# Kernel optimization log

Hardware: AMD Instinct MI355X
Metric: run time of the kernel (lower is better)

The kernel has to match this reference:

```python
import jax, jax.numpy as jnp
import numpy as np

D = 1024  # embed_dim

def setup_inputs() -> dict:
    key = jax.random.key(0)
    ks = jax.random.split(key, 5)
    s = 1.0 / np.sqrt(D)  # keep weight magnitudes sane
    x = jax.random.normal(ks[0], (2, 4096, D), dtype=jnp.float32)
    Wq = jax.random.normal(ks[1], (D, D), dtype=jnp.float32) * s
    Wk = jax.random.normal(ks[2], (D, D), dtype=jnp.float32) * s
    Wv = jax.random.normal(ks[3], (D, D), dtype=jnp.float32) * s
    Wo = jax.random.normal(ks[4], (D, D), dtype=jnp.float32) * s
    return {"x": x, "Wq": Wq, "Wk": Wk, "Wv": Wv, "Wo": Wo}

def reference(x, Wq, Wk, Wv, Wo):
    # torch nn.Linear(no bias): y = x @ W.T
    q = jnp.einsum('bsd,ed->bse', x, Wq)
    k = jnp.einsum('bsd,ed->bse', x, Wk)
    v = jnp.einsum('bsd,ed->bse', x, Wv)
    embed_dim = x.shape[-1]
    scores = jnp.einsum('bqd,bkd->bqk', q, k) / jnp.sqrt(jnp.asarray(embed_dim, x.dtype))
    attn = jax.nn.softmax(scores, axis=-1)  # dropout is identity in eval mode (p=0)
    out = jnp.einsum('bqk,bkd->bqd', attn, v)
    out = jnp.einsum('bsd,ed->bse', out, Wo)
    return out
```

## Files before the change

### kernel.cpp

```cpp
#include <hip/hip_runtime.h>
#include <hip/hip_bf16.h>

using short8 = __attribute__((ext_vector_type(8))) short;
using f32x4  = __attribute__((ext_vector_type(4))) float;

__device__ __forceinline__ unsigned short f2bf(float f) {
  union { float f; unsigned int u; } x; x.f = f;
  unsigned int r = (x.u + 0x7fffu + ((x.u >> 16) & 1u)) >> 16;
  return (unsigned short)r;
}

__device__ __forceinline__ void gld_lds16(const short* gp, short* lp) {
  __builtin_amdgcn_global_load_lds((const __attribute__((address_space(1))) void*)gp,
                                   (__attribute__((address_space(3))) void*)lp, 16, 0, 0);
}

__global__ __launch_bounds__(256) void cast_all(const float* __restrict__ x,
                                                const float* __restrict__ Wq,
                                                const float* __restrict__ Wk,
                                                const float* __restrict__ Wv,
                                                const float* __restrict__ Wo,
                                                short* __restrict__ xb,
                                                short* __restrict__ U,
                                                short* __restrict__ V,
                                                float4* __restrict__ sums4) {
  const int bid = blockIdx.x;
  const int tid = threadIdx.x;
  if (bid < 9216) {
    const float4* src;
    short* dst;
    const int i = bid * 256 + tid;
    if (bid < 8192) {
      src = (const float4*)x + i;
      dst = xb + 4ll * i;
    } else {
      const int off = i - 2097152;
      src = (const float4*)Wo + off;
      dst = U + 1048576 + 4ll * off;
    }
    float4 f = *src;
    short4 o;
    o.x = (short)f2bf(f.x); o.y = (short)f2bf(f.y);
    o.z = (short)f2bf(f.z); o.w = (short)f2bf(f.w);
    *(short4*)dst = o;
    if (bid < 8) sums4[bid * 256 + tid] = float4{0.f, 0.f, 0.f, 0.f};
  } else {
    __shared__ short tls[64][65];
    const int t  = bid - 9216;
    const int w  = t >> 8;
    const int ti = t & 255;
    const int bx = ti & 15, by = ti >> 4;
    const float* src = (w == 0) ? Wq : (w == 1) ? Wk : Wv;
    short* dst = (w == 0) ? V : (w == 1) ? U : V + 1048576;
    const int r  = tid >> 4;
    const int c4 = (tid & 15) * 4;
#pragma unroll
    for (int s = 0; s < 4; ++s) {
      float4 f = *(const float4*)(src + (long long)(by * 64 + r + s * 16) * 1024 + bx * 64 + c4);
      tls[r + s * 16][c4 + 0] = (short)f2bf(f.x);
      tls[r + s * 16][c4 + 1] = (short)f2bf(f.y);
      tls[r + s * 16][c4 + 2] = (short)f2bf(f.z);
      tls[r + s * 16][c4 + 3] = (short)f2bf(f.w);
    }
    __syncthreads();
#pragma unroll
    for (int s = 0; s < 4; ++s) {
      const int a = r + s * 16;
      short4 o;
      o.x = tls[c4 + 0][a]; o.y = tls[c4 + 1][a];
      o.z = tls[c4 + 2][a]; o.w = tls[c4 + 3][a];
      *(short4*)(dst + (long long)(bx * 64 + a) * 1024 + by * 64 + c4) = o;
    }
  }
}

template <int MODE>
__global__ __launch_bounds__(256) void gemm_bt(const short* __restrict__ A,
                                               const short* __restrict__ B,
                                               void* __restrict__ Cv,
                                               float* __restrict__ sums,
                                               int K, int ldc, float scale,
                                               long long aStr, long long bStr,
                                               long long cStr, int gy, int ng) {
  __shared__ short lA[128 * 64];
  __shared__ short lB[128 * 64];
  const int bid = blockIdx.x;
  const int bx  = bid / ng;
  const int g   = bid % ng;
  const int by  = g % gy;
  const long long z = g / gy;
  const int tid = threadIdx.x;
  const int w   = tid >> 6;
  const int l   = tid & 63;
  const int wm  = w >> 1, wn = w & 1;
  const long long tm = (long long)by * 128;
  const long long tn = (long long)bx * 128;
  A += z * aStr;
  B += z * bStr;

  const bool swp = (MODE == 2) ? (bx < 8) : true;

  f32x4 acc[4][4] = {};

  const int lr   = l >> 3;
  const int scw  = ((l & 7) ^ (lr & 7)) * 8;
  const int q4   = l >> 4;
  const int fr   = l & 15;
  const int xr   = fr & 7;

  for (int k0 = 0; k0 < K; k0 += 64) {
#pragma unroll
    for (int t = 0; t < 4; ++t) {
      const int seg = w * 4 + t;
      gld_lds16(A + (tm + seg * 8 + lr) * (long long)K + k0 + scw, &lA[seg * 512]);
      gld_lds16(B + (tn + seg * 8 + lr) * (long long)K + k0 + scw, &lB[seg * 512]);
    }
    __syncthreads();
#pragma unroll
    for (int kk = 0; kk < 64; kk += 32) {
      const int cs = ((((kk >> 3)) + q4) ^ xr) << 3;
      short8 af[4], bfr[4];
#pragma unroll
      for (int i = 0; i < 4; ++i)
        af[i] = *(const short8*)&lA[(wm * 64 + i * 16 + fr) * 64 + cs];
#pragma unroll
      for (int j = 0; j < 4; ++j)
        bfr[j] = *(const short8*)&lB[(wn * 64 + j * 16 + fr) * 64 + cs];
      if (swp) {
#pragma unroll
        for (int i = 0; i < 4; ++i)
#pragma unroll
          for (int j = 0; j < 4; ++j)
            acc[i][j] = __builtin_amdgcn_mfma_f32_16x16x32_bf16(bfr[j], af[i], acc[i][j], 0, 0, 0);
      } else {
#pragma unroll
        for (int i = 0; i < 4; ++i)
#pragma unroll
          for (int j = 0; j < 4; ++j)
            acc[i][j] = __builtin_amdgcn_mfma_f32_16x16x32_bf16(af[i], bfr[j], acc[i][j], 0, 0, 0);
      }
    }
    __syncthreads();
  }

  const int rb = (l >> 4) * 4;

  if (MODE == 1) {
    unsigned short* dst = (unsigned short*)Cv + z * cStr;
#pragma unroll
    for (int i = 0; i < 4; ++i) {
      const long long row = tm + wm * 64 + i * 16 + fr;
#pragma unroll
      for (int j = 0; j < 4; ++j) {
        const long long colb = tn + wn * 64 + j * 16 + rb;
        short4 pk;
        pk.x = (short)f2bf(acc[i][j][0]); pk.y = (short)f2bf(acc[i][j][1]);
        pk.z = (short)f2bf(acc[i][j][2]); pk.w = (short)f2bf(acc[i][j][3]);
        *(short4*)(dst + row * ldc + colb) = pk;
      }
    }
  } else if (MODE == 2) {
    if (swp) {
      unsigned short* dst = (unsigned short*)Cv;
      const int cb0 = (int)tn + wn * 64;
#pragma unroll
      for (int i = 0; i < 4; ++i) {
        const long long row = tm + wm * 64 + i * 16 + fr;
#pragma unroll
        for (int j = 0; j < 4; ++j) {
          const int colb = cb0 + j * 16 + rb;
          short4 pk;
          pk.x = (short)f2bf(acc[i][j][0]); pk.y = (short)f2bf(acc[i][j][1]);
          pk.z = (short)f2bf(acc[i][j][2]); pk.w = (short)f2bf(acc[i][j][3]);
          *(short4*)(dst + row * 1024 + colb) = pk;
        }
      }
    } else {
      unsigned short* dst = (unsigned short*)Cv + 8388608ll;
      const int cb0 = (int)(tn - 1024) + wn * 64;
#pragma unroll
      for (int i = 0; i < 4; ++i)
#pragma unroll
        for (int j = 0; j < 4; ++j) {
          const long long row0 = tm + wm * 64 + i * 16 + rb;
          const long long b = row0 >> 12, s0 = row0 & 4095;
          const int c = cb0 + j * 16 + fr;
          short4 pk;
          pk.x = (short)f2bf(acc[i][j][0]); pk.y = (short)f2bf(acc[i][j][1]);
          pk.z = (short)f2bf(acc[i][j][2]); pk.w = (short)f2bf(acc[i][j][3]);
          *(short4*)(dst + b * 4194304ll + (long long)c * 4096 + s0) = pk;
        }
    }
  } else if (MODE == 4) {
    unsigned short* dst = (unsigned short*)Cv + z * cStr;
    float* sm = sums + z * 4096;
#pragma unroll
    for (int i = 0; i < 4; ++i) {
      const long long row = tm + wm * 64 + i * 16 + fr;
      float rs = 0.f;
#pragma unroll
      for (int j = 0; j < 4; ++j) {
        const long long colb = tn + wn * 64 + j * 16 + rb;
        short4 pk;
        float e0 = __expf(acc[i][j][0] * scale);
        float e1 = __expf(acc[i][j][1] * scale);
        float e2 = __expf(acc[i][j][2] * scale);
        float e3 = __expf(acc[i][j][3] * scale);
        rs += (e0 + e1) + (e2 + e3);
        pk.x = (short)f2bf(e0); pk.y = (short)f2bf(e1);
        pk.z = (short)f2bf(e2); pk.w = (short)f2bf(e3);
        *(short4*)(dst + row * ldc + colb) = pk;
      }
      rs += __shfl_xor(rs, 16);
      rs += __shfl_xor(rs, 32);
      if (l < 16) atomicAdd(sm + tm + wm * 64 + i * 16 + l, rs);
    }
  } else {
    float* dst = (float*)Cv + z * cStr;
    const float* sm = sums + z * 4096;
#pragma unroll
    for (int i = 0; i < 4; ++i) {
      const long long row = tm + wm * 64 + i * 16 + fr;
      const float inv = 1.0f / sm[row];
#pragma unroll
      for (int j = 0; j < 4; ++j) {
        const long long colb = tn + wn * 64 + j * 16 + rb;
        f32x4 o;
        o[0] = acc[i][j][0] * inv; o[1] = acc[i][j][1] * inv;
        o[2] = acc[i][j][2] * inv; o[3] = acc[i][j][3] * inv;
        *(f32x4*)(dst + row * ldc + colb) = o;
      }
    }
  }
}

extern "C" void kernel_launch(void* const* d_in, const int* in_sizes, int n_in,
                              void* d_out, int out_size, void* d_ws, size_t ws_size,
                              hipStream_t stream) {
  const float* x  = (const float*)d_in[0];
  const float* Wq = (const float*)d_in[1];
  const float* Wk = (const float*)d_in[2];
  const float* Wv = (const float*)d_in[3];
  const float* Wo = (const float*)d_in[4];
  float* out = (float*)d_out;

  char* ws = (char*)d_ws;
  short* xb = (short*)ws;
  short* U  = (short*)(ws + (16ll << 20));
  short* V  = (short*)(ws + (20ll << 20));
  short* W2 = (short*)(ws + (24ll << 20));
  short* t  = (short*)(ws + (28ll << 20));
  short* vt = t + 8388608;
  float* sums = (float*)(ws + (60ll << 20));
  short* sc = (short*)(ws + (88ll << 20));

  const bool batched = ws_size >= 159383552ull;
  dim3 blk(256);

  cast_all<<<9984, blk, 0, stream>>>(x, Wq, Wk, Wv, Wo, xb, U, V, (float4*)sums);

  gemm_bt<1><<<8 * 16, blk, 0, stream>>>(U, V, W2, nullptr, 1024, 1024, 1.f,
                                         1048576ll, 1048576ll, 1048576ll, 8, 16);

  gemm_bt<2><<<16 * 64, blk, 0, stream>>>(xb, W2, t, nullptr, 1024, 1024, 1.f,
                                          0, 0, 0, 64, 64);

  if (batched) {
    gemm_bt<4><<<32 * 64, blk, 0, stream>>>(t, xb, sc, sums, 1024, 4096, 0.03125f,
                                            4194304ll, 4194304ll, 16777216ll, 32, 64);
    gemm_bt<6><<<8 * 64, blk, 0, stream>>>(sc, vt, out, sums, 4096, 1024, 1.f,
                                           16777216ll, 4194304ll, 4194304ll, 32, 64);
  } else {
    for (int b = 0; b < 2; ++b) {
      short* tb  = t  + (long long)b * 4194304;
      short* xbb = xb + (long long)b * 4194304;
      short* vb  = vt + (long long)b * 4194304;
      float* ob  = out + (long long)b * 4194304;
      float* smb = sums + (long long)b * 4096;
      gemm_bt<4><<<32 * 32, blk, 0, stream>>>(tb, xbb, sc, smb, 1024, 4096, 0.03125f,
                                              0, 0, 0, 32, 32);
      gemm_bt<6><<<8 * 32, blk, 0, stream>>>(sc, vb, ob, smb, 4096, 1024, 1.f,
                                             0, 0, 0, 32, 32);
    }
  }
}
```

Baseline: 328.7 us.

## Add 256x256-tile 8-wave GEMM kernel for projection and score stages

Introduces a new gemm8 kernel using 512 threads, 256x256 output tiles, a 4-stage LDS ring with direct global-to-LDS loads, and MFMA 16x16x32 bf16. It replaces the 128-tile gemm_bt for the fused projection (MODE 2) and the score/exp stage (MODE 4), with epilogues for bf16 store, transposed V store, and exp with atomic row sums. Larger tiles raise arithmetic intensity and reduce global/LDS traffic per FLOP. The cost is much higher register pressure (128 accumulator floats per thread) and fewer blocks, which may limit occupancy and tail balance.

```diff
diff --git a/kernel.cpp b/kernel.cpp
--- a/kernel.cpp
+++ b/kernel.cpp
@@ -234,6 +234,171 @@
   }
 }
 
+template <int MODE>
+__global__ __launch_bounds__(512, 2) void gemm8(const short* __restrict__ A,
+                                                const short* __restrict__ B,
+                                                void* __restrict__ Cv,
+                                                float* __restrict__ sums,
+                                                int K, int ldc, float scale,
+                                                long long aStr, long long bStr,
+                                                long long cStr, int gy, int ng) {
+  __shared__ __align__(16) short lds[4][2][8192];
+  const int bid = blockIdx.x;
+  const int bx  = bid / ng;
+  const int g   = bid % ng;
+  const int by  = g % gy;
+  const long long z = g / gy;
+  const int tid = threadIdx.x;
+  const int l   = tid & 63;
+  const int w   = tid >> 6;
+  const int wm  = w >> 2, wn = w & 3;
+  const long long tm = (long long)by * 256;
+  const long long tn = (long long)bx * 256;
+  A += z * aStr;
+  B += z * bStr;
+
+  const bool swp = (MODE == 2) ? (bx < 4) : true;
+
+  f32x4 acc[8][4] = {};
+
+  const int i0 = tid, i1 = tid + 512;
+  const int r0 = i0 >> 2, q0 = i0 & 3;
+  const int r1 = i1 >> 2, q1 = i1 & 3;
+  const int sw0 = (q0 ^ ((r0 >> 1) & 3)) * 8;
+  const int sw1 = (q1 ^ ((r1 >> 1) & 3)) * 8;
+  const int db0 = (tid & 448) * 8;
+  const int db1 = 4096 + db0;
+  const short* Arow0 = A + (tm + r0) * (long long)K + sw0;
+  const short* Arow1 = A + (tm + r1) * (long long)K + sw1;
+  const short* Brow0 = B + (tn + r0) * (long long)K + sw0;
+  const short* Brow1 = B + (tn + r1) * (long long)K + sw1;
+
+  const int q4 = l >> 4;
+  const int fr = l & 15;
+  int offA[8], offB[4];
+#pragma unroll
+  for (int i = 0; i < 8; ++i) {
+    const int r = wm * 128 + i * 16 + fr;
+    offA[i] = r * 32 + ((q4 ^ ((r >> 1) & 3)) << 3);
+  }
+#pragma unroll
+  for (int j = 0; j < 4; ++j) {
+    const int r = wn * 64 + j * 16 + fr;
+    offB[j] = r * 32 + ((q4 ^ ((r >> 1) & 3)) << 3);
+  }
+
+  const int nt = K >> 5;
+
+#define STAGE8(tt)                                          \
+  {                                                         \
+    const int s_ = (tt) & 3;                                \
+    const int k_ = (tt) << 5;                               \
+    gld_lds16(Arow0 + k_, &lds[s_][0][db0]);                \
+    gld_lds16(Arow1 + k_, &lds[s_][0][db1]);                \
+    gld_lds16(Brow0 + k_, &lds[s_][1][db0]);                \
+    gld_lds16(Brow1 + k_, &lds[s_][1][db1]);                \
+  }
+
+  STAGE8(0);
+  STAGE8(1);
+  asm volatile("s_waitcnt vmcnt(4)" ::: "memory");
+  __builtin_amdgcn_s_barrier();
+
+  for (int t = 0; t < nt; ++t) {
+    if (t + 2 < nt) STAGE8(t + 2);
+    const short* sA = &lds[t & 3][0][0];
+    const short* sB = &lds[t & 3][1][0];
+    short8 bfr[4];
+#pragma unroll
+    for (int j = 0; j < 4; ++j) bfr[j] = *(const short8*)&sB[offB[j]];
+    __builtin_amdgcn_s_setprio(1);
+    if (swp) {
+#pragma unroll
+      for (int i = 0; i < 8; ++i) {
+        short8 af = *(const short8*)&sA[offA[i]];
+#pragma unroll
+        for (int j = 0; j < 4; ++j)
+          acc[i][j] = __builtin_amdgcn_mfma_f32_16x16x32_bf16(bfr[j], af, acc[i][j], 0, 0, 0);
+      }
+    } else {
+#pragma unroll
+      for (int i = 0; i < 8; ++i) {
+        short8 af = *(const short8*)&sA[offA[i]];
+#pragma unroll
+        for (int j = 0; j < 4; ++j)
+          acc[i][j] = __builtin_amdgcn_mfma_f32_16x16x32_bf16(af, bfr[j], acc[i][j], 0, 0, 0);
+      }
+    }
+    __builtin_amdgcn_s_setprio(0);
+    if (t + 1 < nt) {
+      if (t + 2 < nt) { asm volatile("s_waitcnt vmcnt(4)" ::: "memory"); }
+      else            { asm volatile("s_waitcnt vmcnt(0)" ::: "memory"); }
+      __builtin_amdgcn_s_barrier();
+    }
+  }
+#undef STAGE8
+
+  const int rb = q4 * 4;
+
+  if (MODE == 2) {
+    if (swp) {
+      unsigned short* dst = (unsigned short*)Cv;
+      const int cb0 = (int)tn + wn * 64;
+#pragma unroll
+      for (int i = 0; i < 8; ++i) {
+        const long long row = tm + wm * 128 + i * 16 + fr;
+#pragma unroll
+        for (int j = 0; j < 4; ++j) {
+          const int colb = cb0 + j * 16 + rb;
+          short4 pk;
+          pk.x = (short)f2bf(acc[i][j][0]); pk.y = (short)f2bf(acc[i][j][1]);
+          pk.z = (short)f2bf(acc[i][j][2]); pk.w = (short)f2bf(acc[i][j][3]);
+          *(short4*)(dst + row * 1024 + colb) = pk;
+        }
+      }
+    } else {
+      unsigned short* dst = (unsigned short*)Cv + 8388608ll;
+      const int cb0 = (int)(tn - 1024) + wn * 64;
+#pragma unroll
+      for (int i = 0; i < 8; ++i)
+#pragma unroll
+        for (int j = 0; j < 4; ++j) {
+          const long long row0 = tm + wm * 128 + i * 16 + rb;
+          const long long b = row0 >> 12, s0 = row0 & 4095;
+          const int c = cb0 + j * 16 + fr;
+          short4 pk;
+          pk.x = (short)f2bf(acc[i][j][0]); pk.y = (short)f2bf(acc[i][j][1]);
+          pk.z = (short)f2bf(acc[i][j][2]); pk.w = (short)f2bf(acc[i][j][3]);
+          *(short4*)(dst + b * 4194304ll + (long long)c * 4096 + s0) = pk;
+        }
+    }
+  } else {
+    unsigned short* dst = (unsigned short*)Cv + z * cStr;
+    float* sm = sums + z * 4096;
+#pragma unroll
+    for (int i = 0; i < 8; ++i) {
+      const long long row = tm + wm * 128 + i * 16 + fr;
+      float rs = 0.f;
+#pragma unroll
+      for (int j = 0; j < 4; ++j) {
+        const long long colb = tn + wn * 64 + j * 16 + rb;
+        short4 pk;
+        float e0 = __expf(acc[i][j][0] * scale);
+        float e1 = __expf(acc[i][j][1] * scale);
+        float e2 = __expf(acc[i][j][2] * scale);
+        float e3 = __expf(acc[i][j][3] * scale);
+        rs += (e0 + e1) + (e2 + e3);
+        pk.x = (short)f2bf(e0); pk.y = (short)f2bf(e1);
+        pk.z = (short)f2bf(e2); pk.w = (short)f2bf(e3);
+        *(short4*)(dst + row * ldc + colb) = pk;
+      }
+      rs += __shfl_xor(rs, 16);
+      rs += __shfl_xor(rs, 32);
+      if (l < 16) atomicAdd(sm + tm + wm * 128 + i * 16 + l, rs);
+    }
+  }
+}
+
 extern "C" void kernel_launch(void* const* d_in, const int* in_sizes, int n_in,
                               void* d_out, int out_size, void* d_ws, size_t ws_size,
                               hipStream_t stream) {
@@ -256,18 +421,19 @@
 
   const bool batched = ws_size >= 159383552ull;
   dim3 blk(256);
+  dim3 blk8(512);
 
   cast_all<<<9984, blk, 0, stream>>>(x, Wq, Wk, Wv, Wo, xb, U, V, (float4*)sums);
 
   gemm_bt<1><<<8 * 16, blk, 0, stream>>>(U, V, W2, nullptr, 1024, 1024, 1.f,
                                          1048576ll, 1048576ll, 1048576ll, 8, 16);
 
-  gemm_bt<2><<<16 * 64, blk, 0, stream>>>(xb, W2, t, nullptr, 1024, 1024, 1.f,
-                                          0, 0, 0, 64, 64);
+  gemm8<2><<<8 * 32, blk8, 0, stream>>>(xb, W2, t, nullptr, 1024, 1024, 1.f,
+                                        0, 0, 0, 32, 32);
 
   if (batched) {
-    gemm_bt<4><<<32 * 64, blk, 0, stream>>>(t, xb, sc, sums, 1024, 4096, 0.03125f,
-                                            4194304ll, 4194304ll, 16777216ll, 32, 64);
+    gemm8<4><<<16 * 32, blk8, 0, stream>>>(t, xb, sc, sums, 1024, 4096, 0.03125f,
+                                           4194304ll, 4194304ll, 16777216ll, 16, 32);
     gemm_bt<6><<<8 * 64, blk, 0, stream>>>(sc, vt, out, sums, 4096, 1024, 1.f,
                                            16777216ll, 4194304ll, 4194304ll, 32, 64);
   } else {
@@ -277,8 +443,8 @@
       short* vb  = vt + (long long)b * 4194304;
       float* ob  = out + (long long)b * 4194304;
       float* smb = sums + (long long)b * 4096;
-      gemm_bt<4><<<32 * 32, blk, 0, stream>>>(tb, xbb, sc, smb, 1024, 4096, 0.03125f,
-                                              0, 0, 0, 32, 32);
+      gemm8<4><<<16 * 16, blk8, 0, stream>>>(tb, xbb, sc, smb, 1024, 4096, 0.03125f,
+                                             0, 0, 0, 16, 16);
       gemm_bt<6><<<8 * 32, blk, 0, stream>>>(sc, vb, ob, smb, 4096, 1024, 1.f,
                                              0, 0, 0, 32, 32);
     }
```

Result: slower. 557.2 us (+69.5%).
